# Kernel optimization log

Hardware: AMD Instinct MI355X
Metric: run time of the kernel (lower is better)

Reference implementation:

```python
import math
import jax, jax.numpy as jnp
import numpy as np
from jax.scipy.linalg import solve_triangular

K, D, Q = 512, 2048, 8
B = 8192
EPS = 1e-5
RHO0 = math.log(math.exp(1.0) - 1.0)  # softplus^-1(1.0), matches psi_init=scale_init=1.0


def setup_inputs() -> dict:
    key = jax.random.key(0)
    k1, k2, k3, k4, k5 = jax.random.split(key, 5)
    x = jax.random.normal(k1, (B, D), dtype=jnp.float32)
    mu = jax.random.normal(k2, (K, D), dtype=jnp.float32)          # centroids
    dir_raw = jax.random.normal(k3, (K, D, Q), dtype=jnp.float32) / math.sqrt(D)
    scale_rho = jnp.full((K, Q), RHO0, dtype=jnp.float32) + 0.01 * jax.random.normal(k4, (K, Q), dtype=jnp.float32)
    psi_rho = jnp.full((D,), RHO0, dtype=jnp.float32) + 0.01 * jax.random.normal(k5, (D,), dtype=jnp.float32)
    pi_logits = jnp.zeros((K,), dtype=jnp.float32)
    return {"x": x, "mu": mu, "dir_raw": dir_raw, "scale_rho": scale_rho,
            "psi_rho": psi_rho, "pi_logits": pi_logits}


def _nll(x, mu, dir_raw, scale_rho, psi_rho, pi_logits):
    Dd = x.shape[1]
    q = dir_raw.shape[2]
    # diagonal noise (shared across components since psi_per_component=False)
    psi = jax.nn.softplus(psi_rho) + EPS                      # (D,)
    psi_inv = 1.0 / psi                                       # (D,)
    # factor loadings W_k = normalize(dir_raw, dim=1) * softplus(scale)
    n = jnp.maximum(jnp.linalg.norm(dir_raw, axis=1, keepdims=True), EPS)
    W = (dir_raw / n) * jax.nn.softplus(scale_rho)[:, None, :]  # (K, D, q)
    # Woodbury inner matrix M_k = I + W^T Psi^{-1} W and its Cholesky
    A = W * jnp.sqrt(psi_inv)[None, :, None]                  # (K, D, q)
    M = jnp.einsum('kdi,kdj->kij', A, A) + jnp.eye(q, dtype=W.dtype)[None]
    L = jnp.linalg.cholesky(M)                                # (K, q, q) lower
    # quadratic form pieces
    xT_Pinv_x = (x ** 2) @ psi_inv                            # (B,)
    xT_Pinv_mu = x @ (psi_inv[None, :] * mu).T                # (B, K)
    muT_Pinv_mu = jnp.sum(mu ** 2 * psi_inv[None, :], axis=-1)  # (K,)
    quad_Psi = xT_Pinv_x[:, None] - 2.0 * xT_Pinv_mu + muT_Pinv_mu[None, :]
    PinvW = psi_inv[None, :, None] * W                        # (K, D, q)
    WT_Pinv_x = jnp.einsum('bd,kdq->bkq', x, PinvW)           # (B, K, q)
    WT_Pinv_mu = jnp.einsum('kd,kdq->kq', mu, PinvW)          # (K, q)
    v = WT_Pinv_x - WT_Pinv_mu[None, :, :]                    # (B, K, q)
    # Ez = M^{-1} v via the Cholesky factor (batched over K, rhs over B)
    vT = jnp.transpose(v, (1, 2, 0))                          # (K, q, B)
    y = solve_triangular(L, vT, lower=True)
    EzT = solve_triangular(jnp.swapaxes(L, -1, -2), y, lower=False)
    Ez = jnp.transpose(EzT, (2, 0, 1))                        # (B, K, q)
    quad = quad_Psi - jnp.sum(v * Ez, axis=-1)                # (B, K)
    # log-determinants via Woodbury: log|C| = log|Psi| + log|M|
    logdet_Psi = jnp.sum(jnp.log(psi))                        # scalar (shared psi)
    logdet_M = 2.0 * jnp.sum(jnp.log(jnp.diagonal(L, axis1=-2, axis2=-1)), axis=-1)  # (K,)
    logdet_C = logdet_Psi + logdet_M                          # (K,)
    ll = -0.5 * (Dd * math.log(2.0 * math.pi) + logdet_C[None, :] + quad)  # (B, K)
    log_pi = jax.nn.log_softmax(pi_logits)
    logp = jax.scipy.special.logsumexp(ll + log_pi[None, :], axis=1)  # (B,)
    return jnp.mean(-logp)


def reference(x, mu, dir_raw, scale_rho, psi_rho, pi_logits):
    return _nll(x, mu, dir_raw, scale_rho, psi_rho, pi_logits)
```

## Files before the change

### kernel.cpp

```cpp
#include <hip/hip_runtime.h>

constexpr int Bn = 8192;
constexpr int Dd = 2048;
constexpr int Kk = 512;
constexpr int Qq = 8;
constexpr int Nn = Kk * 9;
constexpr float DLOG2PI = 3763.9722f;

constexpr int BM = 256, BN = 288, BK = 128;
constexpr int NT = Dd / BK;

constexpr float SX = 16.f;
constexpr float SW = 64.f;
constexpr float SG = 16.f;
constexpr float INV_UW = 1.f / (16.f * 64.f);
constexpr float INV_UG = 1.f / (16.f * 16.f);

constexpr size_t OFF_PSI   = 0;
constexpr size_t OFF_LDP   = 8192;
constexpr size_t OFF_LOGPI = 8448;
constexpr size_t OFF_OFFK  = 10752;
constexpr size_t OFF_MINV  = 13056;
constexpr size_t OFF_XPX   = 144384;
constexpr size_t OFF_XBF   = 177408;
constexpr size_t OFF_GT    = 33731840;
constexpr size_t OFF_LL    = 52606208;
constexpr size_t OFF_PART  = 69383424;

constexpr int LDS_BS   = 0;
constexpr int LDS_MINV = 73728;
constexpr int LDS_OFFC = 82048;
constexpr int LDS_CS   = 82176;
constexpr int LDS_TOT  = 157952;

typedef float f32x4 __attribute__((ext_vector_type(4)));
typedef int   i32x4v __attribute__((ext_vector_type(4)));
typedef int   i32x8v __attribute__((ext_vector_type(8)));
typedef __attribute__((address_space(3))) char lds_char;

__device__ inline float softplusf(float x) {
  return fmaxf(x, 0.f) + log1pf(expf(-fabsf(x)));
}
__device__ inline unsigned short f2bf(float x) {
  unsigned int u = __builtin_bit_cast(unsigned int, x);
  u = (u + 0x7fffu + ((u >> 16) & 1u)) >> 16;
  return (unsigned short)u;
}
__device__ inline unsigned int pack2(float a, float b) {
  return (unsigned int)f2bf(a) | ((unsigned int)f2bf(b) << 16);
}
__device__ inline float bf2f(unsigned int u16) {
  unsigned int v = u16 << 16;
  return __builtin_bit_cast(float, v);
}
__device__ inline unsigned char f2fp8(float x) {
  int v = __builtin_amdgcn_cvt_pk_fp8_f32(x, 0.f, 0, false);
  return (unsigned char)(v & 0xff);
}
__device__ inline void glds16(const unsigned char* g, char* l) {
  __builtin_amdgcn_global_load_lds(
      (const __attribute__((address_space(1))) unsigned int*)g,
      (__attribute__((address_space(3))) unsigned int*)l, 16, 0, 0);
}

#define BARRIER()                                   \
  do {                                              \
    asm volatile("" ::: "memory");                  \
    __builtin_amdgcn_s_barrier();                   \
    asm volatile("" ::: "memory");                  \
  } while (0)

#define DSR2(LO, HI, PL, PH, IMMS)                                    \
  asm volatile("ds_read_b128 %0, %2 offset:" IMMS "\n\t"              \
               "ds_read_b128 %1, %3 offset:" IMMS                     \
               : "=&v"(LO), "=&v"(HI)                                 \
               : "v"(PL), "v"(PH));

#define WAITLG(NS)                                                    \
  do {                                                                \
    asm volatile("s_waitcnt lgkmcnt(" NS ")" ::: "memory");           \
    __builtin_amdgcn_sched_barrier(0);                                \
  } while (0)

#define CAT8(D, LO, HI)                                               \
  do { D[0]=LO[0];D[1]=LO[1];D[2]=LO[2];D[3]=LO[3];                   \
       D[4]=HI[0];D[5]=HI[1];D[6]=HI[2];D[7]=HI[3]; } while (0)

__global__ __launch_bounds__(256) void prep_psi(
    const float* __restrict__ psi_rho, const float* __restrict__ pi_logits,
    float* __restrict__ psi_inv, float* __restrict__ logdetPsi,
    float* __restrict__ logpi) {
  __shared__ float red[256];
  int t = threadIdx.x;
  float acc = 0.f;
  for (int d = t; d < Dd; d += 256) {
    float p = softplusf(psi_rho[d]) + 1e-5f;
    psi_inv[d] = 1.f / p;
    acc += logf(p);
  }
  red[t] = acc;
  __syncthreads();
  for (int s = 128; s > 0; s >>= 1) { if (t < s) red[t] += red[t + s]; __syncthreads(); }
  if (t == 0) *logdetPsi = red[0];
  __syncthreads();
  float mx = -3.4e38f;
  for (int i = t; i < Kk; i += 256) mx = fmaxf(mx, pi_logits[i]);
  red[t] = mx;
  __syncthreads();
  for (int s = 128; s > 0; s >>= 1) { if (t < s) red[t] = fmaxf(red[t], red[t + s]); __syncthreads(); }
  mx = red[0];
  __syncthreads();
  float se = 0.f;
  for (int i = t; i < Kk; i += 256) se += expf(pi_logits[i] - mx);
  red[t] = se;
  __syncthreads();
  for (int s = 128; s > 0; s >>= 1) { if (t < s) red[t] += red[t + s]; __syncthreads(); }
  float lse = mx + logf(red[0]);
  for (int i = t; i < Kk; i += 256) logpi[i] = pi_logits[i] - lse;
}

#define TRI(i, j) ((i) * ((i) + 1) / 2 + (j))

__global__ __launch_bounds__(256) void prep_all(
    const float* __restrict__ x, const float* __restrict__ mu,
    const float* __restrict__ dir_raw, const float* __restrict__ scale_rho,
    const float* __restrict__ psi_inv,
    float* __restrict__ offk, float* __restrict__ Minv,
    unsigned char* __restrict__ Gq, unsigned char* __restrict__ xq,
    float* __restrict__ xPx) {
  __shared__ unsigned short sDir[Dd * 8];
  __shared__ float sPwmd[Dd];
  __shared__ float redk[4 * 53];
  __shared__ float R[53];
  __shared__ float sAl[8], sAh[8];
  __shared__ float sLt[36], sLdt[8];

  int bid = blockIdx.x;
  int t = threadIdx.x, lane = t & 63, w = t >> 6;

  if (bid >= Kk) {
    int b = bid - Kk;
    const float4* xr = (const float4*)(x + (size_t)b * Dd);
    const float4* pr = (const float4*)psi_inv;
    float4 v0 = xr[2 * t], v1 = xr[2 * t + 1];
    float4 p0 = pr[2 * t], p1 = pr[2 * t + 1];
    float acc = v0.x * v0.x * p0.x + v0.y * v0.y * p0.y + v0.z * v0.z * p0.z + v0.w * v0.w * p0.w
              + v1.x * v1.x * p1.x + v1.y * v1.y * p1.y + v1.z * v1.z * p1.z + v1.w * v1.w * p1.w;
    unsigned int q0 = (unsigned int)__builtin_amdgcn_cvt_pk_fp8_f32(SX * v0.x, SX * v0.y, 0, false);
    q0 = (unsigned int)__builtin_amdgcn_cvt_pk_fp8_f32(SX * v0.z, SX * v0.w, (int)q0, true);
    unsigned int q1 = (unsigned int)__builtin_amdgcn_cvt_pk_fp8_f32(SX * v1.x, SX * v1.y, 0, false);
    q1 = (unsigned int)__builtin_amdgcn_cvt_pk_fp8_f32(SX * v1.z, SX * v1.w, (int)q1, true);
    uint2 o; o.x = q0; o.y = q1;
    size_t dst = ((size_t)(b >> 4) * 16 + (size_t)(t >> 4)) * 2048
               + (size_t)(((((t & 15) >> 2) << 4) | (b & 15))) * 32
               + (size_t)(t & 3) * 8;
    *(uint2*)(xq + dst) = o;
#pragma unroll
    for (int s2 = 32; s2; s2 >>= 1) acc += __shfl_down(acc, s2, 64);
    float* r4 = sPwmd;
    if (lane == 0) r4[w] = acc;
    __syncthreads();
    if (t == 0) xPx[b] = r4[0] + r4[1] + r4[2] + r4[3];
    return;
  }

  int k = bid;
  float vals[53];
#pragma unroll
  for (int i = 0; i < 53; i++) vals[i] = 0.f;
  const float4* dirp = (const float4*)(dir_raw + (size_t)k * Dd * Qq);
  for (int d = t; d < Dd; d += 256) {
    float4 da = dirp[d * 2], db = dirp[d * 2 + 1];
    float dir8[8] = {da.x, da.y, da.z, da.w, db.x, db.y, db.z, db.w};
    float pw = psi_inv[d];
    float md = mu[(size_t)k * Dd + d];
    int c = 0;
#pragma unroll
    for (int i = 0; i < 8; i++) {
      float dip = dir8[i] * pw;
#pragma unroll
      for (int j = 0; j < 8; j++) {
        if (j < i) continue;
        vals[c] += dip * dir8[j]; c++;
      }
    }
#pragma unroll
    for (int q = 0; q < 8; q++) vals[36 + q] += dir8[q] * dir8[q];
    float mp = md * pw;
#pragma unroll
    for (int q = 0; q < 8; q++) vals[44 + q] += mp * dir8[q];
    vals[52] += md * mp;
    uint4 pk;
    pk.x = pack2(pw * dir8[0], pw * dir8[1]);
    pk.y = pack2(pw * dir8[2], pw * dir8[3]);
    pk.z = pack2(pw * dir8[4], pw * dir8[5]);
    pk.w = pack2(pw * dir8[6], pw * dir8[7]);
    *(uint4*)(sDir + d * 8) = pk;
    sPwmd[d] = mp;
  }
#pragma unroll
  for (int v = 0; v < 53; v++) {
    float val = vals[v];
#pragma unroll
    for (int o = 32; o; o >>= 1) val += __shfl_down(val, o, 64);
    if (lane == 0) redk[w * 53 + v] = val;
  }
  __syncthreads();
  if (t < 53) R[t] = redk[t] + redk[53 + t] + redk[106 + t] + redk[159 + t];
  __syncthreads();
  if (t == 0) {
    float Sf[8][8];
    {
      int c2 = 0;
#pragma unroll
      for (int i = 0; i < 8; i++) {
#pragma unroll
        for (int j = 0; j < 8; j++) {
          if (j < i) continue;
          float v = R[c2++]; Sf[i][j] = v; Sf[j][i] = v;
        }
      }
    }
    float alpha[8];
#pragma unroll
    for (int q = 0; q < 8; q++) {
      float nr = fmaxf(sqrtf(R[36 + q]), 1e-5f);
      alpha[q] = softplusf(scale_rho[(size_t)k * 8 + q]) / nr;
    }
    float Mm[8][8];
#pragma unroll
    for (int i = 0; i < 8; i++)
#pragma unroll
      for (int j = 0; j < 8; j++)
        Mm[i][j] = alpha[i] * alpha[j] * Sf[i][j] + (i == j ? 1.f : 0.f);
    float L[8][8], Ld[8];
#pragma unroll
    for (int i = 0; i < 8; i++) {
#pragma unroll
      for (int j = 0; j < 8; j++) {
        if (j > i) continue;
        float s2 = Mm[i][j];
#pragma unroll
        for (int p = 0; p < 8; p++) { if (p < j) s2 -= L[i][p] * L[j][p]; }
        if (i == j) { L[i][i] = sqrtf(s2); Ld[i] = 1.f / L[i][i]; }
        else        L[i][j] = s2 * Ld[j];
      }
    }
    float logdetM = 0.f;
#pragma unroll
    for (int i = 0; i < 8; i++) logdetM += 2.f * logf(L[i][i]);
    float wv[8];
#pragma unroll
    for (int q = 0; q < 8; q++) wv[q] = alpha[q] * R[44 + q];
    float y[8], h[8];
#pragma unroll
    for (int i = 0; i < 8; i++) {
      float s2 = wv[i];
#pragma unroll
      for (int p = 0; p < 8; p++) { if (p < i) s2 -= L[i][p] * y[p]; }
      y[i] = s2 * Ld[i];
    }
#pragma unroll
    for (int i = 7; i >= 0; i--) {
      float s2 = y[i];
#pragma unroll
      for (int p = 0; p < 8; p++) { if (p > i) s2 -= L[p][i] * h[p]; }
      h[i] = s2 * Ld[i];
    }
    float cc = R[52];
#pragma unroll
    for (int q = 0; q < 8; q++) cc -= wv[q] * h[q];
    {
      int c3 = 0;
#pragma unroll
      for (int i = 0; i < 8; i++)
#pragma unroll
        for (int j = 0; j < 8; j++) { if (j <= i) sLt[c3++] = L[i][j]; }
#pragma unroll
      for (int i = 0; i < 8; i++) sLdt[i] = Ld[i];
    }
    offk[k] = -0.5f * (DLOG2PI + logdetM + cc);
#pragma unroll
    for (int q = 0; q < 8; q++) { sAl[q] = alpha[q]; sAh[q] = alpha[q] * h[q]; }
  }
  __syncthreads();
  if (t < 8) {
    int col = t;
    float yy[8], z[8];
#pragma unroll
    for (int i = 0; i < 8; i++) {
      float s2 = (i == col) ? 1.f : 0.f;
#pragma unroll
      for (int p = 0; p < 8; p++) { if (p < i) s2 -= sLt[TRI(i, p)] * yy[p]; }
      yy[i] = s2 * sLdt[i];
    }
#pragma unroll
    for (int i = 7; i >= 0; i--) {
      float s2 = yy[i];
#pragma unroll
      for (int p = 0; p < 8; p++) { if (p > i) s2 -= sLt[TRI(p, i)] * z[p]; }
      z[i] = s2 * sLdt[i];
    }
#pragma unroll
    for (int r2 = 0; r2 < 8; r2++) Minv[(size_t)k * 64 + r2 * 8 + col] = z[r2];
  }
  float al[8], ah[8];
#pragma unroll
  for (int q = 0; q < 8; q++) { al[q] = sAl[q]; ah[q] = sAh[q]; }
  for (int d = t; d < Dd; d += 256) {
    uint4 pk = *(const uint4*)(sDir + d * 8);
    float pd[8];
    pd[0] = bf2f(pk.x & 0xffffu); pd[1] = bf2f(pk.x >> 16);
    pd[2] = bf2f(pk.y & 0xffffu); pd[3] = bf2f(pk.y >> 16);
    pd[4] = bf2f(pk.z & 0xffffu); pd[5] = bf2f(pk.z >> 16);
    pd[6] = bf2f(pk.w & 0xffffu); pd[7] = bf2f(pk.w >> 16);
    float gs = 0.f;
#pragma unroll
    for (int q = 0; q < 8; q++) {
      Gq[((size_t)(k * 9 + q)) * Dd + d] = f2fp8(SW * al[q] * pd[q]);
      gs += ah[q] * pd[q];
    }
    Gq[((size_t)(k * 9 + 8)) * Dd + d] = f2fp8(SG * (sPwmd[d] - gs));
  }
}

#define MFMA_COL(nt, bv)                                              \
  do {                                                                \
    acc[0][nt] = __builtin_amdgcn_mfma_scale_f32_16x16x128_f8f6f4(    \
        a0, bv, acc[0][nt], 0, 0, 0, 0x7f7f7f7f, 0, 0x7f7f7f7f);      \
    acc[1][nt] = __builtin_amdgcn_mfma_scale_f32_16x16x128_f8f6f4(    \
        a1, bv, acc[1][nt], 0, 0, 0, 0x7f7f7f7f, 0, 0x7f7f7f7f);      \
    acc[2][nt] = __builtin_amdgcn_mfma_scale_f32_16x16x128_f8f6f4(    \
        a2, bv, acc[2][nt], 0, 0, 0, 0x7f7f7f7f, 0, 0x7f7f7f7f);      \
    acc[3][nt] = __builtin_amdgcn_mfma_scale_f32_16x16x128_f8f6f4(    \
        a3, bv, acc[3][nt], 0, 0, 0, 0x7f7f7f7f, 0, 0x7f7f7f7f);      \
  } while (0)

__global__ __launch_bounds__(512, 1) void gemm_ll(
    const unsigned char* __restrict__ xq, const unsigned char* __restrict__ Gq,
    const float* __restrict__ Minv, const float* __restrict__ offk,
    const float* __restrict__ logpi, const float* __restrict__ logdetPsi,
    const float* __restrict__ xPx, float* __restrict__ ll) {
  __shared__ __align__(16) char smem[LDS_TOT];
  float* sMinv = (float*)(smem + LDS_MINV);
  float* sOff  = (float*)(smem + LDS_OFFC);
  float* Cs    = (float*)(smem + LDS_CS);
  lds_char* sm3 = (lds_char*)smem;

  int t = threadIdx.x, lane = t & 63, w = t >> 6;
  int wr = w >> 1, wc = w & 1;
  int m0 = blockIdx.y * BM;
  int n0 = blockIdx.x * BN;
  int comp0 = blockIdx.x * 32;

  for (int i = t; i < 2048; i += 512) {
    int cl = i >> 6, idx = i & 63;
    sMinv[cl * 65 + idx] = Minv[(size_t)comp0 * 64 + i];
  }
  if (t < 32)
    sOff[t] = offk[comp0 + t] + logpi[comp0 + t] - 0.5f * logdetPsi[0];

  f32x4 acc[4][9];
  f32x4 zero = {0.f, 0.f, 0.f, 0.f};
#pragma unroll
  for (int mt = 0; mt < 4; mt++)
#pragma unroll
    for (int nt = 0; nt < 9; nt++) acc[mt][nt] = zero;

  int rr  = lane >> 3;
  int cph = lane & 7;
  int csw = cph ^ rr;
  int quad = lane >> 4, r16 = lane & 15;
  int s8 = r16 & 7;
  int clo = (((2 * quad)     ^ s8) * 16);
  int chi = (((2 * quad + 1) ^ s8) * 16);
  const int boff = (wc * 144 + r16) * 128;
  const unsigned char* aP =
      xq + ((size_t)(blockIdx.y * 16 + wr * 4)) * 32768 + (size_t)lane * 32;

  auto stage = [&](int buf, int k0) {
    char* dst = smem + LDS_BS + buf * 36864;
    if (w < 4) {
#pragma unroll
      for (int i = 0; i < 5; ++i) {
        int j = w * 5 + i;
        glds16(Gq + (size_t)(n0 + j * 8 + rr) * Dd + k0 + csw * 16,
               dst + j * 1024);
      }
    } else {
#pragma unroll
      for (int i = 0; i < 4; ++i) {
        int j = 20 + (w - 4) * 4 + i;
        glds16(Gq + (size_t)(n0 + j * 8 + rr) * Dd + k0 + csw * 16,
               dst + j * 1024);
      }
    }
  };

  i32x8v a0 = *(const i32x8v*)(aP);
  i32x8v a1 = *(const i32x8v*)(aP + 32768);
  i32x8v a2 = *(const i32x8v*)(aP + 65536);
  i32x8v a3 = *(const i32x8v*)(aP + 98304);
  stage(0, 0);
  asm volatile("s_waitcnt vmcnt(0) lgkmcnt(0)" ::: "memory");
  BARRIER();

#pragma unroll 1
  for (int tt = 0; tt < NT; ++tt) {
    int cur = tt & 1;
    lds_char* pBl = sm3 + (LDS_BS + cur * 36864) + boff + clo;
    lds_char* pBh = sm3 + (LDS_BS + cur * 36864) + boff + chi;
    i32x4v bXl, bXh, bYl, bYh, bZl, bZh;
    DSR2(bXl, bXh, pBl, pBh, "0")
    DSR2(bYl, bYh, pBl, pBh, "2048")
    DSR2(bZl, bZh, pBl, pBh, "4096")
    if (tt < NT - 1) stage(cur ^ 1, (tt + 1) * BK);
    i32x8v bq;
    WAITLG("4"); CAT8(bq, bXl, bXh); MFMA_COL(0, bq);
    DSR2(bXl, bXh, pBl, pBh, "6144")
    WAITLG("4"); CAT8(bq, bYl, bYh); MFMA_COL(1, bq);
    DSR2(bYl, bYh, pBl, pBh, "8192")
    WAITLG("4"); CAT8(bq, bZl, bZh); MFMA_COL(2, bq);
    DSR2(bZl, bZh, pBl, pBh, "10240")
    WAITLG("4"); CAT8(bq, bXl, bXh); MFMA_COL(3, bq);
    DSR2(bXl, bXh, pBl, pBh, "12288")
    WAITLG("4"); CAT8(bq, bYl, bYh); MFMA_COL(4, bq);
    DSR2(bYl, bYh, pBl, pBh, "14336")
    WAITLG("4"); CAT8(bq, bZl, bZh); MFMA_COL(5, bq);
    DSR2(bZl, bZh, pBl, pBh, "16384")
    WAITLG("4"); CAT8(bq, bXl, bXh); MFMA_COL(6, bq);
    WAITLG("2"); CAT8(bq, bYl, bYh); MFMA_COL(7, bq);
    WAITLG("0"); CAT8(bq, bZl, bZh); MFMA_COL(8, bq);
    __builtin_amdgcn_sched_barrier(0);
    {
      int kn = (tt + 1) & (NT - 1);
      a0 = *(const i32x8v*)(aP +         (size_t)kn * 2048);
      a1 = *(const i32x8v*)(aP + 32768 + (size_t)kn * 2048);
      a2 = *(const i32x8v*)(aP + 65536 + (size_t)kn * 2048);
      a3 = *(const i32x8v*)(aP + 98304 + (size_t)kn * 2048);
    }
    asm volatile("s_waitcnt vmcnt(8)" ::: "memory");
    BARRIER();
  }

  float P[36];
  {
    const float* Mi = sMinv + (wc * 16 + r16) * 65;
    int c = 0;
#pragma unroll
    for (int i2 = 0; i2 < 8; i2++) {
      P[c++] = 0.5f * Mi[i2 * 8 + i2];
#pragma unroll
      for (int j2 = i2 + 1; j2 < 8; j2++) P[c++] = Mi[i2 * 8 + j2];
    }
  }
  float offc = sOff[wc * 16 + r16];

  float* myC = Cs + w * (16 * 148);
#pragma unroll
  for (int mt = 0; mt < 4; ++mt) {
#pragma unroll
    for (int nt = 0; nt < 9; ++nt) {
#pragma unroll
      for (int r = 0; r < 4; r++) {
        myC[(quad * 4 + r) * 148 + nt * 16 + r16] = acc[mt][nt][r];
      }
    }
#pragma unroll
    for (int i = 0; i < 4; i++) {
      int row_l = quad + 4 * i;
      int b = m0 + wr * 64 + mt * 16 + row_l;
      const float* cp = myC + row_l * 148 + r16 * 9;
      float u[8];
#pragma unroll
      for (int j = 0; j < 8; j++) u[j] = cp[j] * INV_UW;
      float s = cp[8] * INV_UG;
      float tq = 0.f;
      int c = 0;
#pragma unroll
      for (int i2 = 0; i2 < 8; i2++) {
        float s2 = P[c++] * u[i2];
#pragma unroll
        for (int j2 = i2 + 1; j2 < 8; j2++) s2 += P[c++] * u[j2];
        tq += u[i2] * s2;
      }
      ll[(size_t)b * Kk + comp0 + wc * 16 + r16] = offc + s + tq - 0.5f * xPx[b];
    }
  }
}

__global__ __launch_bounds__(256) void lse_rows(
    const float* __restrict__ ll, float* __restrict__ part) {
  int t = threadIdx.x, lane = t & 63, w = t >> 6;
  int b = blockIdx.x * 4 + w;
  const float* row = ll + (size_t)b * Kk;
  float v[8];
  float mx = -3.4e38f;
#pragma unroll
  for (int i = 0; i < 8; i++) { v[i] = row[lane + 64 * i]; mx = fmaxf(mx, v[i]); }
#pragma unroll
  for (int o = 32; o; o >>= 1) mx = fmaxf(mx, __shfl_xor(mx, o, 64));
  float se = 0.f;
#pragma unroll
  for (int i = 0; i < 8; i++) se += expf(v[i] - mx);
#pragma unroll
  for (int o = 32; o; o >>= 1) se += __shfl_xor(se, o, 64);
  __shared__ float r4[4];
  if (lane == 0) r4[w] = -(mx + logf(se));
  __syncthreads();
  if (t == 0) part[blockIdx.x] = r4[0] + r4[1] + r4[2] + r4[3];
}

__global__ __launch_bounds__(256) void final_mean(
    const float* __restrict__ part, float* __restrict__ out) {
  int t = threadIdx.x, lane = t & 63, w = t >> 6;
  float acc = 0.f;
  for (int i = t; i < 2048; i += 256) acc += part[i];
#pragma unroll
  for (int o = 32; o; o >>= 1) acc += __shfl_down(acc, o, 64);
  __shared__ float r4[4];
  if (lane == 0) r4[w] = acc;
  __syncthreads();
  if (t == 0) out[0] = (r4[0] + r4[1] + r4[2] + r4[3]) * (1.0f / 8192.0f);
}

extern "C" void kernel_launch(void* const* d_in, const int* in_sizes, int n_in,
                              void* d_out, int out_size, void* d_ws, size_t ws_size,
                              hipStream_t stream) {
  const float* x         = (const float*)d_in[0];
  const float* mu        = (const float*)d_in[1];
  const float* dir_raw   = (const float*)d_in[2];
  const float* scale_rho = (const float*)d_in[3];
  const float* psi_rho   = (const float*)d_in[4];
  const float* pi_logits = (const float*)d_in[5];
  float* out = (float*)d_out;
  char* ws = (char*)d_ws;

  float* psi_inv          = (float*)(ws + OFF_PSI);
  float* logdetPsi        = (float*)(ws + OFF_LDP);
  float* logpi            = (float*)(ws + OFF_LOGPI);
  float* offk             = (float*)(ws + OFF_OFFK);
  float* Minv             = (float*)(ws + OFF_MINV);
  float* xPx              = (float*)(ws + OFF_XPX);
  unsigned char* xq       = (unsigned char*)(ws + OFF_XBF);
  unsigned char* Gq       = (unsigned char*)(ws + OFF_GT);
  float* ll               = (float*)(ws + OFF_LL);
  float* part             = (float*)(ws + OFF_PART);

  prep_psi<<<1, 256, 0, stream>>>(psi_rho, pi_logits, psi_inv, logdetPsi, logpi);
  prep_all<<<Kk + Bn, 256, 0, stream>>>(x, mu, dir_raw, scale_rho, psi_inv,
                                        offk, Minv, Gq, xq, xPx);
  dim3 g(Nn / BN, Bn / BM);
  gemm_ll<<<g, 512, 0, stream>>>(xq, Gq, Minv, offk, logpi, logdetPsi, xPx, ll);
  lse_rows<<<Bn / 4, 256, 0, stream>>>(ll, part);
  final_mean<<<1, 256, 0, stream>>>(part, out);
}
```

Measured before the change: 233.1 us.

## Split B-tile staging into phases with barriers and MFMA priority boosts

Restructures the main GEMM k-loop: the next-tile global-to-LDS staging is split into two parts interleaved with three phases of LDS reads and MFMA groups, each separated by workgroup barriers, and MFMA blocks run under raised s_setprio. The aim is to keep waves in lockstep so memory issue and matrix math overlap more evenly across the CU. The cost is extra barriers per iteration, full lgkmcnt(0) waits instead of staggered partial waits, and the staging loops are no longer explicitly unrolled.

```diff
diff --git a/kernel.cpp b/kernel.cpp
--- a/kernel.cpp
+++ b/kernel.cpp
@@ -79,6 +79,12 @@
 #define WAITLG(NS)                                                    \
   do {                                                                \
     asm volatile("s_waitcnt lgkmcnt(" NS ")" ::: "memory");           \
+    __builtin_amdgcn_sched_barrier(0);                                \
+  } while (0)
+
+#define WAITVM(NS)                                                    \
+  do {                                                                \
+    asm volatile("s_waitcnt vmcnt(" NS ")" ::: "memory");             \
     __builtin_amdgcn_sched_barrier(0);                                \
   } while (0)
 
@@ -378,18 +384,18 @@
   const unsigned char* aP =
       xq + ((size_t)(blockIdx.y * 16 + wr * 4)) * 32768 + (size_t)lane * 32;
 
-  auto stage = [&](int buf, int k0) {
+  auto stageP = [&](int buf, int k0, int part) {
     char* dst = smem + LDS_BS + buf * 36864;
     if (w < 4) {
-#pragma unroll
-      for (int i = 0; i < 5; ++i) {
+      int i0 = part ? 3 : 0, i1 = part ? 5 : 3;
+      for (int i = i0; i < i1; ++i) {
         int j = w * 5 + i;
         glds16(Gq + (size_t)(n0 + j * 8 + rr) * Dd + k0 + csw * 16,
                dst + j * 1024);
       }
     } else {
-#pragma unroll
-      for (int i = 0; i < 4; ++i) {
+      int i0 = part ? 2 : 0, i1 = part ? 4 : 2;
+      for (int i = i0; i < i1; ++i) {
         int j = 20 + (w - 4) * 4 + i;
         glds16(Gq + (size_t)(n0 + j * 8 + rr) * Dd + k0 + csw * 16,
                dst + j * 1024);
@@ -401,45 +407,60 @@
   i32x8v a1 = *(const i32x8v*)(aP + 32768);
   i32x8v a2 = *(const i32x8v*)(aP + 65536);
   i32x8v a3 = *(const i32x8v*)(aP + 98304);
-  stage(0, 0);
+  stageP(0, 0, 0);
+  stageP(0, 0, 1);
   asm volatile("s_waitcnt vmcnt(0) lgkmcnt(0)" ::: "memory");
   BARRIER();
 
 #pragma unroll 1
   for (int tt = 0; tt < NT; ++tt) {
     int cur = tt & 1;
+    int k1 = (tt + 1) * BK;
+    bool more = (tt < NT - 1);
     lds_char* pBl = sm3 + (LDS_BS + cur * 36864) + boff + clo;
     lds_char* pBh = sm3 + (LDS_BS + cur * 36864) + boff + chi;
     i32x4v bXl, bXh, bYl, bYh, bZl, bZh;
+    i32x8v b0, b1, b2;
     DSR2(bXl, bXh, pBl, pBh, "0")
     DSR2(bYl, bYh, pBl, pBh, "2048")
     DSR2(bZl, bZh, pBl, pBh, "4096")
-    if (tt < NT - 1) stage(cur ^ 1, (tt + 1) * BK);
-    i32x8v bq;
-    WAITLG("4"); CAT8(bq, bXl, bXh); MFMA_COL(0, bq);
+    WAITVM("0");
+    if (more) stageP(cur ^ 1, k1, 0);
+    BARRIER();
+    WAITLG("0");
+    CAT8(b0, bXl, bXh); CAT8(b1, bYl, bYh); CAT8(b2, bZl, bZh);
+    __builtin_amdgcn_s_setprio(1);
+    MFMA_COL(0, b0); MFMA_COL(1, b1); MFMA_COL(2, b2);
+    __builtin_amdgcn_s_setprio(0);
+    BARRIER();
     DSR2(bXl, bXh, pBl, pBh, "6144")
-    WAITLG("4"); CAT8(bq, bYl, bYh); MFMA_COL(1, bq);
     DSR2(bYl, bYh, pBl, pBh, "8192")
-    WAITLG("4"); CAT8(bq, bZl, bZh); MFMA_COL(2, bq);
     DSR2(bZl, bZh, pBl, pBh, "10240")
-    WAITLG("4"); CAT8(bq, bXl, bXh); MFMA_COL(3, bq);
+    if (more) stageP(cur ^ 1, k1, 1);
+    BARRIER();
+    WAITLG("0");
+    CAT8(b0, bXl, bXh); CAT8(b1, bYl, bYh); CAT8(b2, bZl, bZh);
+    __builtin_amdgcn_s_setprio(1);
+    MFMA_COL(3, b0); MFMA_COL(4, b1); MFMA_COL(5, b2);
+    __builtin_amdgcn_s_setprio(0);
+    BARRIER();
     DSR2(bXl, bXh, pBl, pBh, "12288")
-    WAITLG("4"); CAT8(bq, bYl, bYh); MFMA_COL(4, bq);
     DSR2(bYl, bYh, pBl, pBh, "14336")
-    WAITLG("4"); CAT8(bq, bZl, bZh); MFMA_COL(5, bq);
     DSR2(bZl, bZh, pBl, pBh, "16384")
-    WAITLG("4"); CAT8(bq, bXl, bXh); MFMA_COL(6, bq);
-    WAITLG("2"); CAT8(bq, bYl, bYh); MFMA_COL(7, bq);
-    WAITLG("0"); CAT8(bq, bZl, bZh); MFMA_COL(8, bq);
+    BARRIER();
+    WAITLG("0");
+    CAT8(b0, bXl, bXh); CAT8(b1, bYl, bYh); CAT8(b2, bZl, bZh);
+    __builtin_amdgcn_s_setprio(1);
+    MFMA_COL(6, b0); MFMA_COL(7, b1); MFMA_COL(8, b2);
+    __builtin_amdgcn_s_setprio(0);
     __builtin_amdgcn_sched_barrier(0);
-    {
-      int kn = (tt + 1) & (NT - 1);
-      a0 = *(const i32x8v*)(aP +         (size_t)kn * 2048);
-      a1 = *(const i32x8v*)(aP + 32768 + (size_t)kn * 2048);
-      a2 = *(const i32x8v*)(aP + 65536 + (size_t)kn * 2048);
-      a3 = *(const i32x8v*)(aP + 98304 + (size_t)kn * 2048);
-    }
-    asm volatile("s_waitcnt vmcnt(8)" ::: "memory");
+    if (more) {
+      a0 = *(const i32x8v*)(aP +         (size_t)k1 * 16);
+      a1 = *(const i32x8v*)(aP + 32768 + (size_t)k1 * 16);
+      a2 = *(const i32x8v*)(aP + 65536 + (size_t)k1 * 16);
+      a3 = *(const i32x8v*)(aP + 98304 + (size_t)k1 * 16);
+      WAITVM("4");
+    }
     BARRIER();
   }
 
```

Measured after the change: 388.7 us. 66.7% more time.
